# Optimization experiments

Hardware: AMD Instinct MI355X
Metric: run time of the kernel (lower is better)

Reference implementation:

```python
import jax, jax.numpy as jnp
import numpy as np

DIMS = 1024
HEADS = 16
DEPTH = DIMS // HEADS


def setup_inputs() -> dict:
    key = jax.random.key(0)
    kq, kk, kv = jax.random.split(key, 3)
    B, S = 2, 2048
    q = jax.random.normal(kq, (B, S, DIMS), dtype=jnp.float32)
    k = jax.random.normal(kk, (B, S, DIMS), dtype=jnp.float32)
    v = jax.random.normal(kv, (B, S, DIMS), dtype=jnp.float32)
    return {"q": q, "k": k, "v": v}


def _split_heads(x):
    # [B, S, dims] -> [B, heads, S, depth]
    b, s, _ = x.shape
    return x.reshape(b, s, HEADS, DEPTH).transpose(0, 2, 1, 3)


def reference(q, k, v):
    b, s, _ = q.shape
    qh = _split_heads(q)  # [b, h, sq, d]
    kh = _split_heads(k)  # [b, h, sk, d]
    vh = _split_heads(v)  # [b, h, sk, d]
    # keras.layers.Attention default: UNSCALED dot-product scores
    scores = jnp.einsum("bhqd,bhkd->bhqk", qh, kh)
    weights = jax.nn.softmax(scores, axis=-1)
    out = jnp.einsum("bhqk,bhkd->bhqd", weights, vh)
    # merge heads: [b, h, sq, d] -> [b, sq, dims]
    out = out.transpose(0, 2, 1, 3).reshape(b, s, DIMS)
    return out
```

## Files before the change

kernel.cpp:

```cpp
#include <hip/hip_runtime.h>

#define SEQ 2048
#define HEADS 16
#define DEPTH 64
#define DIMS 1024
#define LOG2E 1.44269504088896340736f

typedef _Float16 f16x8 __attribute__((ext_vector_type(8)));
typedef __fp16 fp16v2 __attribute__((ext_vector_type(2)));
typedef float f32x16 __attribute__((ext_vector_type(16)));

__device__ __forceinline__ f32x16 mfma32(f16x8 a, f16x8 b, f32x16 c) {
  return __builtin_amdgcn_mfma_f32_32x32x16_f16(a, b, c, 0, 0, 0);
}

#if __has_builtin(__builtin_amdgcn_exp2f)
#define EXP2(x) __builtin_amdgcn_exp2f(x)
#else
#define EXP2(x) exp2f(x)
#endif

__device__ __forceinline__ unsigned pkbits(float a, float b) {
  union { fp16v2 h; unsigned u; } cv;
  cv.h = __builtin_amdgcn_cvt_pkrtz(a, b);
  return cv.u;
}

#define GLOAD_LDS(g, l)                                                        \
  __builtin_amdgcn_global_load_lds(                                            \
      (const __attribute__((address_space(1))) unsigned int*)(g),              \
      (__attribute__((address_space(3))) unsigned int*)(l), 16, 0, 0)

__global__ __launch_bounds__(256) void prep_kv(const float* __restrict__ k,
                                               const float* __restrict__ v,
                                               _Float16* __restrict__ khf,
                                               _Float16* __restrict__ vtp) {
  const int bid = blockIdx.x;
  if (bid < 2048) {
    int t = bid * 256 + threadIdx.x;
    size_t flat = (size_t)t * 8;
    int b = (int)(flat >> 21);
    int rem = (int)(flat & ((1u << 21) - 1));
    int s = rem >> 10;
    int c = rem & 1023;
    int h = c >> 6;
    int d = c & 63;
    float4 a0 = *(const float4*)(k + flat);
    float4 a1 = *(const float4*)(k + flat + 4);
    float f[8] = {a0.x, a0.y, a0.z, a0.w, a1.x, a1.y, a1.z, a1.w};
    f16x8 th;
    #pragma unroll
    for (int j = 0; j < 8; ++j) th[j] = (_Float16)f[j];
    size_t o = ((size_t)(b * HEADS + h) * SEQ + s) * DEPTH + d;
    *(f16x8*)(khf + o) = th;
  } else {
    int t = (bid - 2048) * 256 + threadIdx.x;
    int d = t & 63;
    int sg = (t >> 6) & 255;
    int bh = t >> 14;
    int b = bh >> 4, h = bh & 15;
    int s0 = sg * 8;
    const float* src = v + ((size_t)(b * SEQ + s0)) * DIMS + h * DEPTH + d;
    _Float16* dst = vtp + ((size_t)bh * DEPTH + d) * SEQ + s0;
    f16x8 tv;
    #pragma unroll
    for (int i = 0; i < 8; ++i) tv[i] = (_Float16)src[(size_t)i * DIMS];
    *(f16x8*)dst = tv;
  }
}

__global__ __launch_bounds__(256, 2) void attn_fwd(
    const float* __restrict__ q, const _Float16* __restrict__ kh,
    const _Float16* __restrict__ vt, float* __restrict__ out) {
  __shared__ _Float16 Kl[2][64 * 64];
  __shared__ _Float16 Vl[2][64 * 64];

  const int tid = threadIdx.x;
  const int w = tid >> 6;
  const int l = tid & 63;
  const int q32 = l & 31;
  const int hi = l >> 5;

  const int bid = blockIdx.x;
  const int wg = (bid & 7) * 64 + (bid >> 3);
  const int qt = wg & 15;
  const int bh = wg >> 4;
  const int b = bh >> 4;
  const int h = bh & 15;

  const int qb = qt * 128 + w * 32;
  const int hoff = h * DEPTH;
  const size_t kvoff = (size_t)bh * SEQ * DEPTH;

  f16x8 qf[4];
  {
    const float* gq = q + (size_t)(b * SEQ + qb + q32) * DIMS + hoff + 8 * hi;
    #pragma unroll
    for (int c = 0; c < 4; ++c) {
      float4 a0 = *(const float4*)(gq + 16 * c);
      float4 a1 = *(const float4*)(gq + 16 * c + 4);
      float f[8] = {a0.x, a0.y, a0.z, a0.w, a1.x, a1.y, a1.z, a1.w};
      f16x8 t;
      #pragma unroll
      for (int j = 0; j < 8; ++j) t[j] = (_Float16)(f[j] * LOG2E);
      qf[c] = t;
    }
  }

  const int srow = l >> 3;
  const int scol = ((l & 7) ^ srow) * 8;
  const _Float16* gk0 = kh + kvoff + (size_t)(16 * w + srow) * DEPTH + scol;
  const _Float16* gv0 = vt + kvoff + (size_t)(16 * w + srow) * SEQ + scol;

  const int x7 = q32 & 7;
  int off[4];
  #pragma unroll
  for (int i = 0; i < 4; ++i) off[i] = ((2 * i + hi) ^ x7) * 8;

  f32x16 acc0 = {}, acc1 = {};
  float mrow = -3e38f;
  float den = 0.f;

  auto stage = [&](int buf, int t) {
    const _Float16* gk = gk0 + (size_t)t * 64 * DEPTH;
    const _Float16* gv = gv0 + (size_t)t * 64;
    GLOAD_LDS(gk, &Kl[buf][(16 * w) * 64]);
    GLOAD_LDS(gk + 8 * DEPTH, &Kl[buf][(16 * w + 8) * 64]);
    GLOAD_LDS(gv, &Vl[buf][(16 * w) * 64]);
    GLOAD_LDS(gv + (size_t)8 * SEQ, &Vl[buf][(16 * w + 8) * 64]);
  };

  auto compute = [&](int buf) {
    f32x16 st0 = {}, st1 = {};
    __builtin_amdgcn_s_setprio(1);
    #pragma unroll
    for (int c = 0; c < 4; ++c) {
      f16x8 kf0 = *(const f16x8*)&Kl[buf][q32 * 64 + off[c]];
      f16x8 kf1 = *(const f16x8*)&Kl[buf][(32 + q32) * 64 + off[c]];
      st0 = mfma32(kf0, qf[c], st0);
      st1 = mfma32(kf1, qf[c], st1);
    }
    __builtin_amdgcn_s_setprio(0);

    float mx = fmaxf(st0[0], st1[0]);
    #pragma unroll
    for (int r = 1; r < 16; ++r) mx = fmaxf(mx, fmaxf(st0[r], st1[r]));
    if (!__all(mx - mrow <= 8.0f)) {
      mx = fmaxf(mx, __shfl_xor(mx, 32));
      float mnew = fmaxf(mrow, mx);
      float sc = EXP2(mrow - mnew);
      mrow = mnew;
      den *= sc;
      #pragma unroll
      for (int r = 0; r < 16; ++r) {
        const int crow = (r & 3) + 8 * (r >> 2) + 4 * hi;
        float scb = __shfl(sc, crow);
        acc0[r] *= scb;
        acc1[r] *= scb;
      }
    }
    float p0[16], p1[16];
    float rs = 0.f;
    #pragma unroll
    for (int r = 0; r < 16; ++r) {
      p0[r] = EXP2(st0[r] - mrow);
      p1[r] = EXP2(st1[r] - mrow);
      rs += p0[r] + p1[r];
    }
    rs += __shfl_xor(rs, 32);
    den += rs;

    f16x8 pa[4];
    auto mkpa = [&](const float* pp, f16x8* dst) {
      #pragma unroll
      for (int sl = 0; sl < 2; ++sl) {
        unsigned x0 = pkbits(pp[8 * sl + 0], pp[8 * sl + 1]);
        unsigned x1 = pkbits(pp[8 * sl + 2], pp[8 * sl + 3]);
        unsigned y0 = pkbits(pp[8 * sl + 4], pp[8 * sl + 5]);
        unsigned y1 = pkbits(pp[8 * sl + 6], pp[8 * sl + 7]);
        asm("v_permlane32_swap_b32 %0, %1" : "+v"(x0), "+v"(y0));
        asm("v_permlane32_swap_b32 %0, %1" : "+v"(x1), "+v"(y1));
        union { unsigned u[4]; f16x8 v; } pu;
        pu.u[0] = x0; pu.u[1] = x1; pu.u[2] = y0; pu.u[3] = y1;
        dst[sl] = pu.v;
      }
    };
    mkpa(p0, &pa[0]);
    mkpa(p1, &pa[2]);

    __builtin_amdgcn_s_setprio(1);
    #pragma unroll
    for (int s = 0; s < 4; ++s) {
      f16x8 vf0 = *(const f16x8*)&Vl[buf][q32 * 64 + off[s]];
      f16x8 vf1 = *(const f16x8*)&Vl[buf][(32 + q32) * 64 + off[s]];
      acc0 = mfma32(pa[s], vf0, acc0);
      acc1 = mfma32(pa[s], vf1, acc1);
    }
    __builtin_amdgcn_s_setprio(0);
  };

  stage(0, 0);
  __syncthreads();
  #pragma unroll 1
  for (int kt = 0; kt < SEQ / 64; kt += 2) {
    stage(1, kt + 1);
    compute(0);
    __syncthreads();
    if (kt + 2 < SEQ / 64) stage(0, kt + 2);
    compute(1);
    __syncthreads();
  }

  #pragma unroll
  for (int r = 0; r < 16; ++r) {
    const int crow = (r & 3) + 8 * (r >> 2) + 4 * hi;
    float dn = __shfl(den, crow);
    float rden = 1.0f / dn;
    float* po = out + (size_t)(b * SEQ + qb + crow) * DIMS + hoff;
    po[q32] = acc0[r] * rden;
    po[32 + q32] = acc1[r] * rden;
  }
}

extern "C" void kernel_launch(void* const* d_in, const int* in_sizes, int n_in,
                              void* d_out, int out_size, void* d_ws, size_t ws_size,
                              hipStream_t stream) {
  const float* q = (const float*)d_in[0];
  const float* k = (const float*)d_in[1];
  const float* v = (const float*)d_in[2];
  float* out = (float*)d_out;

  const size_t tsz = (size_t)2 * HEADS * SEQ * DEPTH;
  _Float16* khf = (_Float16*)d_ws;
  _Float16* vtp = khf + tsz;

  prep_kv<<<4096, 256, 0, stream>>>(k, v, khf, vtp);
  attn_fwd<<<512, 256, 0, stream>>>(q, khf, vtp, out);
}
```

Measured before the change: 72.57 us.

## Software-pipeline QK^T one tile ahead, triple-buffer V, compute softmax denominator via MFMA

```diff
diff --git a/kernel.cpp b/kernel.cpp
--- a/kernel.cpp
+++ b/kernel.cpp
@@ -73,7 +73,7 @@
     const float* __restrict__ q, const _Float16* __restrict__ kh,
     const _Float16* __restrict__ vt, float* __restrict__ out) {
   __shared__ _Float16 Kl[2][64 * 64];
-  __shared__ _Float16 Vl[2][64 * 64];
+  __shared__ _Float16 Vl[3][64 * 64];
 
   const int tid = threadIdx.x;
   const int w = tid >> 6;
@@ -107,41 +107,53 @@
     }
   }
 
-  const int srow = l >> 3;
-  const int scol = ((l & 7) ^ srow) * 8;
-  const _Float16* gk0 = kh + kvoff + (size_t)(16 * w + srow) * DEPTH + scol;
-  const _Float16* gv0 = vt + kvoff + (size_t)(16 * w + srow) * SEQ + scol;
-
-  const int x7 = q32 & 7;
+  const int j8 = l >> 3;
+  const int sch0 = (l & 7) ^ j8 ^ ((2 * w) & 3);
+  const int sch1 = sch0 ^ 1;
+  const _Float16* gkA = kh + kvoff + (size_t)(16 * w + j8) * DEPTH + sch0 * 8;
+  const _Float16* gkB =
+      kh + kvoff + (size_t)(16 * w + 8 + j8) * DEPTH + sch1 * 8;
+  const _Float16* gvA = vt + kvoff + (size_t)(16 * w + j8) * SEQ + sch0 * 8;
+  const _Float16* gvB =
+      vt + kvoff + (size_t)(16 * w + 8 + j8) * SEQ + sch1 * 8;
+
+  const int mask0 = (q32 & 7) ^ ((q32 >> 3) & 3);
   int off[4];
   #pragma unroll
-  for (int i = 0; i < 4; ++i) off[i] = ((2 * i + hi) ^ x7) * 8;
+  for (int c = 0; c < 4; ++c) off[c] = ((2 * c + hi) ^ mask0) * 8;
 
   f32x16 acc0 = {}, acc1 = {};
+  f32x16 dacc = {};
   float mrow = -3e38f;
-  float den = 0.f;
-
-  auto stage = [&](int buf, int t) {
-    const _Float16* gk = gk0 + (size_t)t * 64 * DEPTH;
-    const _Float16* gv = gv0 + (size_t)t * 64;
-    GLOAD_LDS(gk, &Kl[buf][(16 * w) * 64]);
-    GLOAD_LDS(gk + 8 * DEPTH, &Kl[buf][(16 * w + 8) * 64]);
-    GLOAD_LDS(gv, &Vl[buf][(16 * w) * 64]);
-    GLOAD_LDS(gv + (size_t)8 * SEQ, &Vl[buf][(16 * w + 8) * 64]);
+
+  const f16x8 onesf = {1, 1, 1, 1, 1, 1, 1, 1};
+
+  auto stage = [&](int kb, int vb, int t) {
+    const _Float16* gk1 = gkA + (size_t)t * 64 * DEPTH;
+    const _Float16* gk2 = gkB + (size_t)t * 64 * DEPTH;
+    const _Float16* gv1 = gvA + t * 64;
+    const _Float16* gv2 = gvB + t * 64;
+    GLOAD_LDS(gk1, &Kl[kb][(16 * w) * 64]);
+    GLOAD_LDS(gk2, &Kl[kb][(16 * w + 8) * 64]);
+    GLOAD_LDS(gv1, &Vl[vb][(16 * w) * 64]);
+    GLOAD_LDS(gv2, &Vl[vb][(16 * w + 8) * 64]);
   };
 
-  auto compute = [&](int buf) {
-    f32x16 st0 = {}, st1 = {};
+  auto qkt = [&](int kb, f32x16& s0, f32x16& s1) {
+    f32x16 z = {};
+    s0 = z; s1 = z;
     __builtin_amdgcn_s_setprio(1);
     #pragma unroll
     for (int c = 0; c < 4; ++c) {
-      f16x8 kf0 = *(const f16x8*)&Kl[buf][q32 * 64 + off[c]];
-      f16x8 kf1 = *(const f16x8*)&Kl[buf][(32 + q32) * 64 + off[c]];
-      st0 = mfma32(kf0, qf[c], st0);
-      st1 = mfma32(kf1, qf[c], st1);
+      f16x8 kf0 = *(const f16x8*)&Kl[kb][q32 * 64 + off[c]];
+      f16x8 kf1 = *(const f16x8*)&Kl[kb][(32 + q32) * 64 + off[c]];
+      s0 = mfma32(kf0, qf[c], s0);
+      s1 = mfma32(kf1, qf[c], s1);
     }
     __builtin_amdgcn_s_setprio(0);
-
+  };
+
+  auto smax_pv = [&](f32x16& st0, f32x16& st1, int vb) {
     float mx = fmaxf(st0[0], st1[0]);
     #pragma unroll
     for (int r = 1; r < 16; ++r) mx = fmaxf(mx, fmaxf(st0[r], st1[r]));
@@ -150,25 +162,21 @@
       float mnew = fmaxf(mrow, mx);
       float sc = EXP2(mrow - mnew);
       mrow = mnew;
-      den *= sc;
       #pragma unroll
       for (int r = 0; r < 16; ++r) {
         const int crow = (r & 3) + 8 * (r >> 2) + 4 * hi;
         float scb = __shfl(sc, crow);
         acc0[r] *= scb;
         acc1[r] *= scb;
+        dacc[r] *= scb;
       }
     }
     float p0[16], p1[16];
-    float rs = 0.f;
     #pragma unroll
     for (int r = 0; r < 16; ++r) {
       p0[r] = EXP2(st0[r] - mrow);
       p1[r] = EXP2(st1[r] - mrow);
-      rs += p0[r] + p1[r];
-    }
-    rs += __shfl_xor(rs, 32);
-    den += rs;
+    }
 
     f16x8 pa[4];
     auto mkpa = [&](const float* pp, f16x8* dst) {
@@ -191,31 +199,41 @@
     __builtin_amdgcn_s_setprio(1);
     #pragma unroll
     for (int s = 0; s < 4; ++s) {
-      f16x8 vf0 = *(const f16x8*)&Vl[buf][q32 * 64 + off[s]];
-      f16x8 vf1 = *(const f16x8*)&Vl[buf][(32 + q32) * 64 + off[s]];
+      f16x8 vf0 = *(const f16x8*)&Vl[vb][q32 * 64 + off[s]];
+      f16x8 vf1 = *(const f16x8*)&Vl[vb][(32 + q32) * 64 + off[s]];
       acc0 = mfma32(pa[s], vf0, acc0);
       acc1 = mfma32(pa[s], vf1, acc1);
+      dacc = mfma32(pa[s], onesf, dacc);
     }
     __builtin_amdgcn_s_setprio(0);
   };
 
-  stage(0, 0);
+  f32x16 stA0, stA1, stB0, stB1;
+  stage(0, 0, 0);
   __syncthreads();
+  stage(1, 1, 1);
+  qkt(0, stA0, stA1);
+  __syncthreads();
+  int va = 0;
   #pragma unroll 1
-  for (int kt = 0; kt < SEQ / 64; kt += 2) {
-    stage(1, kt + 1);
-    compute(0);
+  for (int t = 0; t < SEQ / 64; t += 2) {
+    const int v1 = va == 2 ? 0 : va + 1;
+    const int v2 = v1 == 2 ? 0 : v1 + 1;
+    if (t + 2 < SEQ / 64) stage(0, v2, t + 2);
+    qkt(1, stB0, stB1);
+    smax_pv(stA0, stA1, va);
     __syncthreads();
-    if (kt + 2 < SEQ / 64) stage(0, kt + 2);
-    compute(1);
+    if (t + 3 < SEQ / 64) stage(1, va, t + 3);
+    if (t + 2 < SEQ / 64) qkt(0, stA0, stA1);
+    smax_pv(stB0, stB1, v1);
     __syncthreads();
+    va = v2;
   }
 
   #pragma unroll
   for (int r = 0; r < 16; ++r) {
     const int crow = (r & 3) + 8 * (r >> 2) + 4 * hi;
-    float dn = __shfl(den, crow);
-    float rden = 1.0f / dn;
+    float rden = 1.0f / dacc[r];
     float* po = out + (size_t)(b * SEQ + qb + crow) * DIMS + hoff;
     po[q32] = acc0[r] * rden;
     po[32 + q32] = acc1[r] * rden;
```

Result: faster. 70.58 us (-2.7%).

## Give each wave private K/V LDS buffers, drop block barriers, compute rowsum via MFMA

Applied to the files above, without the earlier changes.

```diff
diff --git a/kernel.cpp b/kernel.cpp
--- a/kernel.cpp
+++ b/kernel.cpp
@@ -5,6 +5,7 @@
 #define DEPTH 64
 #define DIMS 1024
 #define LOG2E 1.44269504088896340736f
+#define NTILES 64
 
 typedef _Float16 f16x8 __attribute__((ext_vector_type(8)));
 typedef __fp16 fp16v2 __attribute__((ext_vector_type(2)));
@@ -30,6 +31,12 @@
   __builtin_amdgcn_global_load_lds(                                            \
       (const __attribute__((address_space(1))) unsigned int*)(g),              \
       (__attribute__((address_space(3))) unsigned int*)(l), 16, 0, 0)
+
+#define WAITC(n)                                                               \
+  do {                                                                         \
+    asm volatile("s_waitcnt vmcnt(" #n ")" ::: "memory");                      \
+    __builtin_amdgcn_sched_barrier(0);                                         \
+  } while (0)
 
 __global__ __launch_bounds__(256) void prep_kv(const float* __restrict__ k,
                                                const float* __restrict__ v,
@@ -72,8 +79,7 @@
 __global__ __launch_bounds__(256, 2) void attn_fwd(
     const float* __restrict__ q, const _Float16* __restrict__ kh,
     const _Float16* __restrict__ vt, float* __restrict__ out) {
-  __shared__ _Float16 Kl[2][64 * 64];
-  __shared__ _Float16 Vl[2][64 * 64];
+  __shared__ _Float16 lds[4][2][4096];
 
   const int tid = threadIdx.x;
   const int w = tid >> 6;
@@ -107,115 +113,123 @@
     }
   }
 
-  const int srow = l >> 3;
-  const int scol = ((l & 7) ^ srow) * 8;
-  const _Float16* gk0 = kh + kvoff + (size_t)(16 * w + srow) * DEPTH + scol;
-  const _Float16* gv0 = vt + kvoff + (size_t)(16 * w + srow) * SEQ + scol;
-
-  const int x7 = q32 & 7;
-  int off[4];
-  #pragma unroll
-  for (int i = 0; i < 4; ++i) off[i] = ((2 * i + hi) ^ x7) * 8;
+  const int j8 = l >> 3;
+  const int j4 = l >> 2;
+  const _Float16* gkp[4];
+  const _Float16* gvp[4];
+  #pragma unroll
+  for (int i = 0; i < 4; ++i) {
+    gkp[i] = kh + kvoff + (size_t)(8 * i + j8) * DEPTH +
+             (((l & 7) ^ j8 ^ (i & 3)) * 8);
+    gvp[i] = vt + kvoff + (size_t)(16 * i + (j4 & 15)) * SEQ +
+             (((l & 3) ^ (j4 & 3)) * 8);
+  }
+
+  const int kmask = (q32 & 7) ^ ((q32 >> 3) & 3);
+  int koff[4];
+  #pragma unroll
+  for (int c = 0; c < 4; ++c) koff[c] = q32 * 64 + ((2 * c + hi) ^ kmask) * 8;
+  const int vmask = q32 & 3;
+  int voff0[2], voff1[2];
+  #pragma unroll
+  for (int s = 0; s < 2; ++s) {
+    const int ch = (2 * s + hi) ^ vmask;
+    voff0[s] = 2048 + q32 * 32 + ch * 8;
+    voff1[s] = 2048 + (32 + q32) * 32 + ch * 8;
+  }
 
   f32x16 acc0 = {}, acc1 = {};
+  f32x16 dacc = {};
   float mrow = -3e38f;
-  float den = 0.f;
+
+  const f16x8 onesf = {1, 1, 1, 1, 1, 1, 1, 1};
 
   auto stage = [&](int buf, int t) {
-    const _Float16* gk = gk0 + (size_t)t * 64 * DEPTH;
-    const _Float16* gv = gv0 + (size_t)t * 64;
-    GLOAD_LDS(gk, &Kl[buf][(16 * w) * 64]);
-    GLOAD_LDS(gk + 8 * DEPTH, &Kl[buf][(16 * w + 8) * 64]);
-    GLOAD_LDS(gv, &Vl[buf][(16 * w) * 64]);
-    GLOAD_LDS(gv + (size_t)8 * SEQ, &Vl[buf][(16 * w + 8) * 64]);
+    _Float16* base = &lds[w][buf][0];
+    #pragma unroll
+    for (int i = 0; i < 4; ++i)
+      GLOAD_LDS(gkp[i] + (size_t)t * 32 * DEPTH, base + i * 512);
+    #pragma unroll
+    for (int i = 0; i < 4; ++i)
+      GLOAD_LDS(gvp[i] + t * 32, base + 2048 + i * 512);
   };
 
   auto compute = [&](int buf) {
-    f32x16 st0 = {}, st1 = {};
+    const _Float16* base = &lds[w][buf][0];
+    f32x16 st = {};
     __builtin_amdgcn_s_setprio(1);
     #pragma unroll
     for (int c = 0; c < 4; ++c) {
-      f16x8 kf0 = *(const f16x8*)&Kl[buf][q32 * 64 + off[c]];
-      f16x8 kf1 = *(const f16x8*)&Kl[buf][(32 + q32) * 64 + off[c]];
-      st0 = mfma32(kf0, qf[c], st0);
-      st1 = mfma32(kf1, qf[c], st1);
+      f16x8 kf = *(const f16x8*)(base + koff[c]);
+      st = mfma32(kf, qf[c], st);
     }
     __builtin_amdgcn_s_setprio(0);
 
-    float mx = fmaxf(st0[0], st1[0]);
-    #pragma unroll
-    for (int r = 1; r < 16; ++r) mx = fmaxf(mx, fmaxf(st0[r], st1[r]));
+    float mx = fmaxf(st[0], st[1]);
+    #pragma unroll
+    for (int r = 2; r < 16; ++r) mx = fmaxf(mx, st[r]);
     if (!__all(mx - mrow <= 8.0f)) {
       mx = fmaxf(mx, __shfl_xor(mx, 32));
       float mnew = fmaxf(mrow, mx);
       float sc = EXP2(mrow - mnew);
       mrow = mnew;
-      den *= sc;
       #pragma unroll
       for (int r = 0; r < 16; ++r) {
         const int crow = (r & 3) + 8 * (r >> 2) + 4 * hi;
         float scb = __shfl(sc, crow);
         acc0[r] *= scb;
         acc1[r] *= scb;
+        dacc[r] *= scb;
       }
     }
-    float p0[16], p1[16];
-    float rs = 0.f;
-    #pragma unroll
-    for (int r = 0; r < 16; ++r) {
-      p0[r] = EXP2(st0[r] - mrow);
-      p1[r] = EXP2(st1[r] - mrow);
-      rs += p0[r] + p1[r];
-    }
-    rs += __shfl_xor(rs, 32);
-    den += rs;
-
-    f16x8 pa[4];
-    auto mkpa = [&](const float* pp, f16x8* dst) {
-      #pragma unroll
-      for (int sl = 0; sl < 2; ++sl) {
-        unsigned x0 = pkbits(pp[8 * sl + 0], pp[8 * sl + 1]);
-        unsigned x1 = pkbits(pp[8 * sl + 2], pp[8 * sl + 3]);
-        unsigned y0 = pkbits(pp[8 * sl + 4], pp[8 * sl + 5]);
-        unsigned y1 = pkbits(pp[8 * sl + 6], pp[8 * sl + 7]);
-        asm("v_permlane32_swap_b32 %0, %1" : "+v"(x0), "+v"(y0));
-        asm("v_permlane32_swap_b32 %0, %1" : "+v"(x1), "+v"(y1));
-        union { unsigned u[4]; f16x8 v; } pu;
-        pu.u[0] = x0; pu.u[1] = x1; pu.u[2] = y0; pu.u[3] = y1;
-        dst[sl] = pu.v;
-      }
-    };
-    mkpa(p0, &pa[0]);
-    mkpa(p1, &pa[2]);
+    #pragma unroll
+    for (int r = 0; r < 16; ++r) st[r] = EXP2(st[r] - mrow);
+
+    f16x8 pa[2];
+    #pragma unroll
+    for (int sl = 0; sl < 2; ++sl) {
+      unsigned x0 = pkbits(st[8 * sl + 0], st[8 * sl + 1]);
+      unsigned x1 = pkbits(st[8 * sl + 2], st[8 * sl + 3]);
+      unsigned y0 = pkbits(st[8 * sl + 4], st[8 * sl + 5]);
+      unsigned y1 = pkbits(st[8 * sl + 6], st[8 * sl + 7]);
+      asm("v_permlane32_swap_b32 %0, %1" : "+v"(x0), "+v"(y0));
+      asm("v_permlane32_swap_b32 %0, %1" : "+v"(x1), "+v"(y1));
+      union { unsigned u[4]; f16x8 v; } pu;
+      pu.u[0] = x0; pu.u[1] = x1; pu.u[2] = y0; pu.u[3] = y1;
+      pa[sl] = pu.v;
+    }
 
     __builtin_amdgcn_s_setprio(1);
     #pragma unroll
-    for (int s = 0; s < 4; ++s) {
-      f16x8 vf0 = *(const f16x8*)&Vl[buf][q32 * 64 + off[s]];
-      f16x8 vf1 = *(const f16x8*)&Vl[buf][(32 + q32) * 64 + off[s]];
+    for (int s = 0; s < 2; ++s) {
+      f16x8 vf0 = *(const f16x8*)(base + voff0[s]);
+      f16x8 vf1 = *(const f16x8*)(base + voff1[s]);
       acc0 = mfma32(pa[s], vf0, acc0);
       acc1 = mfma32(pa[s], vf1, acc1);
+      dacc = mfma32(pa[s], onesf, dacc);
     }
     __builtin_amdgcn_s_setprio(0);
   };
 
   stage(0, 0);
-  __syncthreads();
   #pragma unroll 1
-  for (int kt = 0; kt < SEQ / 64; kt += 2) {
-    stage(1, kt + 1);
+  for (int t = 0; t < NTILES; t += 2) {
+    stage(1, t + 1);
+    WAITC(8);
     compute(0);
-    __syncthreads();
-    if (kt + 2 < SEQ / 64) stage(0, kt + 2);
+    if (t + 2 < NTILES) {
+      stage(0, t + 2);
+      WAITC(8);
+    } else {
+      WAITC(0);
+    }
     compute(1);
-    __syncthreads();
   }
 
   #pragma unroll
   for (int r = 0; r < 16; ++r) {
     const int crow = (r & 3) + 8 * (r >> 2) + 4 * hi;
-    float dn = __shfl(den, crow);
-    float rden = 1.0f / dn;
+    float rden = 1.0f / dacc[r];
     float* po = out + (size_t)(b * SEQ + qb + crow) * DIMS + hoff;
     po[q32] = acc0[r] * rden;
     po[32 + q32] = acc1[r] * rden;
```

After: 81.37 us. 1.12x slower.
